# Kernel optimization log

Hardware: AMD Instinct MI355X
Metric: run time of the kernel (lower is better)

Reference implementation:

```python
import jax, jax.numpy as jnp
import numpy as np

NI, ND, NH = 128, 32, 4  # feature dim, head dim, n heads


def setup_inputs() -> dict:
    key = jax.random.key(0)
    ks = jax.random.split(key, 8)
    nb, nloc, nnei = 2, 1024, 120
    g1 = jax.random.normal(ks[0], (nb, nloc, NI), dtype=jnp.float32)
    gg1 = jax.random.normal(ks[1], (nb, nloc, nnei, NI), dtype=jnp.float32)
    nlist_mask = jax.random.randint(ks[2], (nb, nloc, nnei), 0, 2) > 0
    sw = jax.random.uniform(ks[3], (nb, nloc, nnei), dtype=jnp.float32)
    s = 1.0 / np.sqrt(NI)
    Wq = jax.random.normal(ks[4], (NI, ND * NH), dtype=jnp.float32) * s
    Wkv = jax.random.normal(ks[5], (NI, (ND + NI) * NH), dtype=jnp.float32) * s
    Wh = jax.random.normal(ks[6], (NI * NH, NI), dtype=jnp.float32) * (1.0 / np.sqrt(NI * NH))
    bh = jax.random.normal(ks[7], (NI,), dtype=jnp.float32) * 0.01
    return {"g1": g1, "gg1": gg1, "nlist_mask": nlist_mask, "sw": sw,
            "Wq": Wq, "Wkv": Wkv, "Wh": Wh, "bh": bh}


def reference(g1, gg1, nlist_mask, sw, Wq, Wkv, Wh, bh):
    nb, nloc, nnei = nlist_mask.shape
    # q: [nb, nloc, nh, nd]
    q = (g1 @ Wq).reshape(nb, nloc, ND, NH).transpose(0, 1, 3, 2)
    # kv: [nb, nloc, nh, nnei, nd+ni]
    kv = (gg1 @ Wkv).reshape(nb, nloc, nnei, ND + NI, NH).transpose(0, 1, 4, 2, 3)
    k = kv[..., :ND]   # [nb, nloc, nh, nnei, nd]
    v = kv[..., ND:]   # [nb, nloc, nh, nnei, ni]
    # attention logits over neighbors: [nb, nloc, nh, nnei]
    attnw = jnp.einsum("blhd,blhjd->blhj", q, k) / np.sqrt(ND).astype(np.float32)
    mask = nlist_mask[:, :, None, :]  # [nb, nloc, 1, nnei]
    attnw = jnp.where(mask, attnw, -jnp.inf)
    attnw = jax.nn.softmax(attnw, axis=-1)
    attnw = jnp.where(mask, attnw, 0.0)
    attnw = attnw * sw[:, :, None, :]  # smoothing weight
    ret = jnp.einsum("blhj,blhji->blhi", attnw, v).reshape(nb, nloc, NH * NI)
    return ret @ Wh + bh
```

## Files before the change

kernel.cpp:

```cpp
#include <hip/hip_runtime.h>
#include <math.h>

#define NI   128
#define ND   32
#define NH   4
#define NNEI 120
#define KVW  640
#define NCOL 512

template<int CTRL>
__device__ __forceinline__ float dppf(float x) {
    return __int_as_float(__builtin_amdgcn_update_dpp(
        0, __float_as_int(x), CTRL, 0xF, 0xF, true));
}
__device__ __forceinline__ float red16_sum(float x) {
    x += dppf<0xB1>(x);
    x += dppf<0x4E>(x);
    x += dppf<0x141>(x);
    x += dppf<0x140>(x);
    return x;
}
__device__ __forceinline__ float red16_max(float x) {
    x = fmaxf(x, dppf<0xB1>(x));
    x = fmaxf(x, dppf<0x4E>(x));
    x = fmaxf(x, dppf<0x141>(x));
    x = fmaxf(x, dppf<0x140>(x));
    return x;
}

__global__ __launch_bounds__(256)
void precompute_MP(const float* __restrict__ Wq, const float* __restrict__ Wkv,
                   const float* __restrict__ Wh, float* __restrict__ M2, float* __restrict__ P2)
{
    int idx = blockIdx.x * 256 + threadIdx.x;
    if (idx < NI * NCOL) {
        int i  = idx & 127;
        int h  = (idx >> 7) & 3;
        int i2 = idx >> 9;
        float acc = 0.f;
        #pragma unroll 8
        for (int d = 0; d < ND; ++d)
            acc += Wq[i2 * NI + d * NH + h] * Wkv[i * KVW + d * NH + h];
        M2[i2 * NCOL + h * NI + i] = acc * 0.17677669529663687f;
    } else {
        int j  = idx - NI * NCOL;
        int io = j & 127;
        int i  = (j >> 7) & 127;
        int h  = j >> 14;
        float acc = 0.f;
        #pragma unroll 8
        for (int iv = 0; iv < NI; ++iv)
            acc += Wkv[i * KVW + (ND + iv) * NH + h] * Wh[(h * NI + iv) * NI + io];
        P2[j] = acc;
    }
}

template<int BM, int BN, int BK, int TM, int TN, bool BIAS>
__global__ __launch_bounds__(256)
void gemm_kernel(const float* __restrict__ A, const float* __restrict__ B,
                 const float* __restrict__ bias, float* __restrict__ C,
                 int M, int N, int K)
{
    __shared__ float As[BK][BM + 4];
    __shared__ float Bs[BK][BN + 4];
    const int tid = threadIdx.x;
    const int nbx = N / BN;
    const int bx = blockIdx.x % nbx, by = blockIdx.x / nbx;
    const int m0 = by * BM, n0 = bx * BN;
    const int tx = tid & 15, ty = tid >> 4;

    constexpr int LA = BM * BK / (4 * 256);
    constexpr int LB = BK * BN / (4 * 256);
    constexpr int AF4 = BK / 4;
    constexpr int BF4 = BN / 4;

    float acc[TM][TN] = {};

    for (int k0 = 0; k0 < K; k0 += BK) {
        #pragma unroll
        for (int p = 0; p < LA; ++p) {
            int u  = tid + p * 256;
            int r  = u / AF4;
            int c4 = u % AF4;
            float4 v = *(const float4*)(A + (size_t)(m0 + r) * K + k0 + c4 * 4);
            As[c4 * 4 + 0][r] = v.x;
            As[c4 * 4 + 1][r] = v.y;
            As[c4 * 4 + 2][r] = v.z;
            As[c4 * 4 + 3][r] = v.w;
        }
        #pragma unroll
        for (int p = 0; p < LB; ++p) {
            int u  = tid + p * 256;
            int kk = u / BF4;
            int c4 = u % BF4;
            float4 v = *(const float4*)(B + (size_t)(k0 + kk) * N + n0 + c4 * 4);
            *(float4*)&Bs[kk][c4 * 4] = v;
        }
        __syncthreads();
        #pragma unroll
        for (int kk = 0; kk < BK; ++kk) {
            float a[TM], b[TN];
            if constexpr (TM == 4) {
                float4 a4 = *(const float4*)&As[kk][ty * 4];
                a[0] = a4.x; a[1] = a4.y; a[2] = a4.z; a[3] = a4.w;
            } else {
                #pragma unroll
                for (int m = 0; m < TM; ++m) a[m] = As[kk][ty * TM + m];
            }
            if constexpr (TN == 4) {
                float4 b4 = *(const float4*)&Bs[kk][tx * 4];
                b[0] = b4.x; b[1] = b4.y; b[2] = b4.z; b[3] = b4.w;
            } else {
                #pragma unroll
                for (int n = 0; n < TN; ++n) b[n] = Bs[kk][tx * TN + n];
            }
            #pragma unroll
            for (int m = 0; m < TM; ++m)
                #pragma unroll
                for (int n = 0; n < TN; ++n)
                    acc[m][n] += a[m] * b[n];
        }
        __syncthreads();
    }
    #pragma unroll
    for (int m = 0; m < TM; ++m) {
        int mm = m0 + ty * TM + m;
        #pragma unroll
        for (int n = 0; n < TN; ++n) {
            int nn = n0 + tx * TN + n;
            C[(size_t)mm * N + nn] = acc[m][n] + (BIAS ? bias[nn] : 0.f);
        }
    }
}

__device__ __forceinline__ bool load_mask(const void* p, int is_i32, int idx) {
    if (is_i32) return ((const int*)p)[idx] != 0;
    return ((const unsigned char*)p)[idx] != 0;
}

__global__ __launch_bounds__(256, 3)
void atten_kernel(const float* __restrict__ gg1, const float* __restrict__ qW_all,
                  const void* __restrict__ mask_raw, const float* __restrict__ sw,
                  const float* __restrict__ P2, const float* __restrict__ bh,
                  float* __restrict__ out)
{
    __shared__ float  s_sm[NH][NNEI];
    __shared__ float4 s_part2[16][NH][33];
    __shared__ float4 s_t4[NH][32];
    __shared__ int    s_is_i32;

    const int tid  = threadIdx.x;
    const int bl   = blockIdx.x;
    const int w    = tid >> 6;
    const int lane = tid & 63;
    const int q    = lane >> 4;
    const int c    = lane & 15;

    if (tid < 64) {
        unsigned v = ((const unsigned*)mask_raw)[tid];
        unsigned long long b = __ballot(v <= 1u);
        if (tid == 0) s_is_i32 = (b == 0xFFFFFFFFFFFFFFFFull) ? 1 : 0;
    }

    const int j0 = lane, j1 = lane + 64;
    const int j1c = (j1 < NNEI) ? j1 : 0;
    float sw0 = sw[bl * NNEI + j0];
    float sw1 = (j1 < NNEI) ? sw[bl * NNEI + j1] : 0.f;
    unsigned mraw0_i = ((const int*)mask_raw)[bl * NNEI + j0];
    unsigned mraw1_i = ((const int*)mask_raw)[bl * NNEI + j1c];
    unsigned mraw0_b = ((const unsigned char*)mask_raw)[bl * NNEI + j0];
    unsigned mraw1_b = ((const unsigned char*)mask_raw)[bl * NNEI + j1c];

    const float4* gbase = (const float4*)(gg1 + (size_t)bl * NNEI * NI);
    float4 rgA[8], rgB[8];
    #pragma unroll
    for (int t = 0; t < 8; ++t) {
        int j  = 16 * t + 4 * q + w;
        int jc = (j < NNEI) ? j : 0;
        rgA[t] = gbase[jc * 32 + c];
        rgB[t] = gbase[jc * 32 + c + 16];
    }

    const float4* qwbase = (const float4*)(qW_all + (size_t)bl * NCOL);
    float4 qwA[NH], qwB[NH];
    #pragma unroll
    for (int h = 0; h < NH; ++h) {
        qwA[h] = qwbase[h * 32 + c];
        qwB[h] = qwbase[h * 32 + c + 16];
    }

    #pragma unroll
    for (int t = 0; t < 8; ++t) {
        float4 gA = rgA[t], gB = rgB[t];
        float s0, s1, s2, s3;
        s0 = qwA[0].x*gA.x + qwA[0].y*gA.y + qwA[0].z*gA.z + qwA[0].w*gA.w
           + qwB[0].x*gB.x + qwB[0].y*gB.y + qwB[0].z*gB.z + qwB[0].w*gB.w;
        s1 = qwA[1].x*gA.x + qwA[1].y*gA.y + qwA[1].z*gA.z + qwA[1].w*gA.w
           + qwB[1].x*gB.x + qwB[1].y*gB.y + qwB[1].z*gB.z + qwB[1].w*gB.w;
        s2 = qwA[2].x*gA.x + qwA[2].y*gA.y + qwA[2].z*gA.z + qwA[2].w*gA.w
           + qwB[2].x*gB.x + qwB[2].y*gB.y + qwB[2].z*gB.z + qwB[2].w*gB.w;
        s3 = qwA[3].x*gA.x + qwA[3].y*gA.y + qwA[3].z*gA.z + qwA[3].w*gA.w
           + qwB[3].x*gB.x + qwB[3].y*gB.y + qwB[3].z*gB.z + qwB[3].w*gB.w;
        s0 = red16_sum(s0);
        s1 = red16_sum(s1);
        s2 = red16_sum(s2);
        s3 = red16_sum(s3);
        int j = 16 * t + 4 * q + w;
        if (c == 0 && j < NNEI) {
            s_sm[0][j] = s0;
            s_sm[1][j] = s1;
            s_sm[2][j] = s2;
            s_sm[3][j] = s3;
        }
    }
    __syncthreads();

    {
        const int is32 = s_is_i32;
        bool m0 = is32 ? (mraw0_i != 0u) : ((mraw0_b & 0xFFu) != 0u);
        bool m1 = (j1 < NNEI) && (is32 ? (mraw1_i != 0u) : ((mraw1_b & 0xFFu) != 0u));
        float v0 = m0 ? s_sm[w][j0] : -INFINITY;
        float v1 = m1 ? s_sm[w][j1c] : -INFINITY;

        float mx = fmaxf(v0, v1);
        mx = red16_max(mx);
        mx = fmaxf(mx, __shfl_xor(mx, 16));
        mx = fmaxf(mx, __shfl_xor(mx, 32));

        float e0 = 0.f, e1 = 0.f;
        if (mx != -INFINITY) {
            e0 = m0 ? __expf(v0 - mx) : 0.f;
            e1 = m1 ? __expf(v1 - mx) : 0.f;
        }
        float s = e0 + e1;
        s = red16_sum(s);
        s += __shfl_xor(s, 16);
        s += __shfl_xor(s, 32);
        float inv = (s > 0.f) ? (1.f / s) : 0.f;

        s_sm[w][j0] = e0 * inv * sw0;
        if (j1 < NNEI) s_sm[w][j1] = e1 * inv * sw1;
    }
    __syncthreads();

    {
        float4 aA[NH] = {}, aB[NH] = {};
        #pragma unroll
        for (int t = 0; t < 8; ++t) {
            int j = 16 * t + 4 * q + w;
            bool val = (j < NNEI);
            float4 gA = rgA[t], gB = rgB[t];
            #pragma unroll
            for (int h = 0; h < NH; ++h) {
                float a = val ? s_sm[h][j] : 0.f;
                aA[h].x += a * gA.x; aA[h].y += a * gA.y;
                aA[h].z += a * gA.z; aA[h].w += a * gA.w;
                aB[h].x += a * gB.x; aB[h].y += a * gB.y;
                aB[h].z += a * gB.z; aB[h].w += a * gB.w;
            }
        }
        #pragma unroll
        for (int h = 0; h < NH; ++h) {
            s_part2[w * 4 + q][h][c]      = aA[h];
            s_part2[w * 4 + q][h][c + 16] = aB[h];
        }
    }
    __syncthreads();

    if (tid < 128) {
        int h = tid >> 5, cc = tid & 31;
        float4 r = {0.f, 0.f, 0.f, 0.f};
        #pragma unroll
        for (int g = 0; g < 16; ++g) {
            float4 v = s_part2[g][h][cc];
            r.x += v.x; r.y += v.y; r.z += v.z; r.w += v.w;
        }
        s_t4[h][cc] = r;
    }
    __syncthreads();

    {
        const int io4 = tid & 31, g = tid >> 5;
        float4 oacc = {0.f, 0.f, 0.f, 0.f};
        const float4* P2_4 = (const float4*)P2;
        const float*  s_tf = (const float*)s_t4;
        #pragma unroll 8
        for (int it = 0; it < 64; ++it) {
            int kk = it * 8 + g;
            float4 p = P2_4[kk * 32 + io4];
            float tv = s_tf[kk];
            oacc.x += tv * p.x; oacc.y += tv * p.y;
            oacc.z += tv * p.z; oacc.w += tv * p.w;
        }
        float4* s_pp = &s_part2[0][0][0];
        s_pp[g * 33 + io4] = oacc;
    }
    __syncthreads();
    if (tid < 32) {
        const float4* s_pp = &s_part2[0][0][0];
        float4 r = {0.f, 0.f, 0.f, 0.f};
        #pragma unroll
        for (int g = 0; g < 8; ++g) {
            float4 v = s_pp[g * 33 + tid];
            r.x += v.x; r.y += v.y; r.z += v.z; r.w += v.w;
        }
        float4 b = ((const float4*)bh)[tid];
        r.x += b.x; r.y += b.y; r.z += b.z; r.w += b.w;
        ((float4*)out)[(size_t)bl * 32 + tid] = r;
    }
}

__global__ __launch_bounds__(256, 2)
void fused_fallback(const float* __restrict__ g1, const float* __restrict__ gg1,
                    const void* __restrict__ mask_raw, const float* __restrict__ sw,
                    const float* __restrict__ M2, const float* __restrict__ P2,
                    const float* __restrict__ bh, float* __restrict__ out)
{
    __shared__ float s_gg[NNEI * 129];
    __shared__ float s_qW[NH][NI];
    __shared__ float s_attn[NH][NNEI];
    __shared__ float s_t[NH][NI];
    __shared__ float s_part[2][NI];
    __shared__ int   s_is_i32;

    const int tid = threadIdx.x;
    const int bl  = blockIdx.x;

    if (tid < 64) {
        unsigned v = ((const unsigned*)mask_raw)[tid];
        unsigned long long b = __ballot(v <= 1u);
        if (tid == 0) s_is_i32 = (b == 0xFFFFFFFFFFFFFFFFull) ? 1 : 0;
    }
    {
        const float4* gsrc = (const float4*)(gg1 + (size_t)bl * NNEI * NI);
        #pragma unroll
        for (int p = 0; p < 15; ++p) {
            int u = tid + p * 256;
            int r = u >> 5, c4 = u & 31;
            float4 v = gsrc[u];
            float* dst = &s_gg[r * 129 + c4 * 4];
            dst[0] = v.x; dst[1] = v.y; dst[2] = v.z; dst[3] = v.w;
        }
    }
    {
        const float* g1r = g1 + bl * NI;
        #pragma unroll
        for (int p = 0; p < 2; ++p) {
            int o = tid + p * 256;
            int i = o & (NI - 1);
            int h = o >> 7;
            const float* Mp = M2 + h * NI + i;
            float acc = 0.f;
            #pragma unroll 8
            for (int i2 = 0; i2 < NI; ++i2) acc += g1r[i2] * Mp[i2 * NCOL];
            s_qW[h][i] = acc;
        }
    }
    __syncthreads();
    {
        const int lane = tid & 63, h = tid >> 6;
        const int j0 = lane, j1 = lane + 64;
        const int j1c = (j1 < NNEI) ? j1 : 0;
        const float* row0 = &s_gg[j0 * 129];
        const float* row1 = &s_gg[j1c * 129];
        float dot0 = 0.f, dot1 = 0.f;
        #pragma unroll 8
        for (int i = 0; i < NI; ++i) {
            float w = s_qW[h][i];
            dot0 += row0[i] * w;
            dot1 += row1[i] * w;
        }
        bool m0 = load_mask(mask_raw, s_is_i32, bl * NNEI + j0);
        bool m1 = (j1 < NNEI) && load_mask(mask_raw, s_is_i32, bl * NNEI + j1c);
        float v0 = m0 ? dot0 : -INFINITY;
        float v1 = m1 ? dot1 : -INFINITY;
        float mx = fmaxf(v0, v1);
        #pragma unroll
        for (int off = 32; off; off >>= 1) mx = fmaxf(mx, __shfl_xor(mx, off));
        float e0 = 0.f, e1 = 0.f;
        if (mx != -INFINITY) {
            e0 = m0 ? __expf(v0 - mx) : 0.f;
            e1 = m1 ? __expf(v1 - mx) : 0.f;
        }
        float s = e0 + e1;
        #pragma unroll
        for (int off = 32; off; off >>= 1) s += __shfl_xor(s, off);
        float inv = (s > 0.f) ? (1.f / s) : 0.f;
        s_attn[h][j0] = e0 * inv * sw[bl * NNEI + j0];
        if (j1 < NNEI) s_attn[h][j1] = e1 * inv * sw[bl * NNEI + j1];
    }
    __syncthreads();
    #pragma unroll
    for (int p = 0; p < 2; ++p) {
        int o = tid + p * 256;
        int i = o & (NI - 1);
        int h = o >> 7;
        float acc = 0.f;
        #pragma unroll 8
        for (int j = 0; j < NNEI; ++j) acc += s_attn[h][j] * s_gg[j * 129 + i];
        s_t[h][i] = acc;
    }
    __syncthreads();
    {
        int io = tid & (NI - 1);
        int half = tid >> 7;
        float acc = 0.f;
        #pragma unroll 2
        for (int h = half * 2; h < half * 2 + 2; ++h) {
            const float* Pp = P2 + h * NI * NI + io;
            #pragma unroll 8
            for (int i = 0; i < NI; ++i) acc += s_t[h][i] * Pp[i * NI];
        }
        s_part[half][io] = acc;
    }
    __syncthreads();
    if (tid < NI)
        out[bl * NI + tid] = s_part[0][tid] + s_part[1][tid] + bh[tid];
}

extern "C" void kernel_launch(void* const* d_in, const int* in_sizes, int n_in,
                              void* d_out, int out_size, void* d_ws, size_t ws_size,
                              hipStream_t stream) {
    const float* g1   = (const float*)d_in[0];
    const float* gg1  = (const float*)d_in[1];
    const void*  mask = d_in[2];
    const float* sw   = (const float*)d_in[3];
    const float* Wq   = (const float*)d_in[4];
    const float* Wkv  = (const float*)d_in[5];
    const float* Wh   = (const float*)d_in[6];
    const float* bh   = (const float*)d_in[7];
    float* out = (float*)d_out;

    const int nbl = in_sizes[0] / NI;
    const size_t nM = (size_t)NI * NCOL;
    const size_t nP = (size_t)NCOL * NI;
    const size_t nQ = (size_t)nbl * NCOL;

    float* M2 = (float*)d_ws;
    float* P2 = M2 + nM;

    precompute_MP<<<512, 256, 0, stream>>>(Wq, Wkv, Wh, M2, P2);

    if (ws_size >= (nM + nP + nQ) * sizeof(float)) {
        float* qW = P2 + nP;
        gemm_kernel<64, 64, 32, 4, 4, false>
            <<<(nbl / 64) * (NCOL / 64), 256, 0, stream>>>(g1, M2, nullptr, qW, nbl, NCOL, NI);
        atten_kernel<<<nbl, 256, 0, stream>>>(gg1, qW, mask, sw, P2, bh, out);
    } else {
        fused_fallback<<<nbl, 256, 0, stream>>>(g1, gg1, mask, sw, M2, P2, bh, out);
    }
}
```

Measured before the change: 56.52 us.

## Process two atoms per attention block and fuse P2 precompute into qW GEMM

The attention kernel now handles two atoms per block. Each P2 float4 load in the output projection is reused for both atoms, and the second atom's gg1 rows are loaded while the first is being reduced. The precompute is split: M2 gets its own small kernel, and the P2 computation moves into extra blocks of the qW GEMM launch so it runs alongside the GEMM. The cost is half as many attention blocks, which lowers parallelism across CUs, and the main path is now hard-coded to nbl==2048.

```diff
diff --git a/kernel.cpp b/kernel.cpp
--- a/kernel.cpp
+++ b/kernel.cpp
@@ -26,6 +26,21 @@
     x = fmaxf(x, dppf<0x141>(x));
     x = fmaxf(x, dppf<0x140>(x));
     return x;
+}
+
+__global__ __launch_bounds__(256)
+void precompute_M2(const float* __restrict__ Wq, const float* __restrict__ Wkv,
+                   float* __restrict__ M2)
+{
+    int idx = blockIdx.x * 256 + threadIdx.x;
+    int i  = idx & 127;
+    int h  = (idx >> 7) & 3;
+    int i2 = idx >> 9;
+    float acc = 0.f;
+    #pragma unroll 8
+    for (int d = 0; d < ND; ++d)
+        acc += Wq[i2 * NI + d * NH + h] * Wkv[i * KVW + d * NH + h];
+    M2[i2 * NCOL + h * NI + i] = acc * 0.17677669529663687f;
 }
 
 __global__ __launch_bounds__(256)
@@ -55,82 +70,86 @@
     }
 }
 
-template<int BM, int BN, int BK, int TM, int TN, bool BIAS>
+#define G1_BM 64
+#define G1_BN 64
+#define G1_BK 32
 __global__ __launch_bounds__(256)
-void gemm_kernel(const float* __restrict__ A, const float* __restrict__ B,
-                 const float* __restrict__ bias, float* __restrict__ C,
-                 int M, int N, int K)
-{
-    __shared__ float As[BK][BM + 4];
-    __shared__ float Bs[BK][BN + 4];
+void gemm1_p2(const float* __restrict__ g1, const float* __restrict__ M2,
+              const float* __restrict__ Wkv, const float* __restrict__ Wh,
+              float* __restrict__ qW, float* __restrict__ P2)
+{
+    __shared__ float As[G1_BK][G1_BM + 4];
+    __shared__ float Bs[G1_BK][G1_BN + 4];
     const int tid = threadIdx.x;
-    const int nbx = N / BN;
+
+    if (blockIdx.x >= 256) {
+        int j  = (blockIdx.x - 256) * 256 + tid;
+        int io = j & 127;
+        int i  = (j >> 7) & 127;
+        int h  = j >> 14;
+        float acc = 0.f;
+        #pragma unroll 8
+        for (int iv = 0; iv < NI; ++iv)
+            acc += Wkv[i * KVW + (ND + iv) * NH + h] * Wh[(h * NI + iv) * NI + io];
+        P2[j] = acc;
+        return;
+    }
+
+    const int nbx = NCOL / G1_BN;
     const int bx = blockIdx.x % nbx, by = blockIdx.x / nbx;
-    const int m0 = by * BM, n0 = bx * BN;
+    const int m0 = by * G1_BM, n0 = bx * G1_BN;
     const int tx = tid & 15, ty = tid >> 4;
-
-    constexpr int LA = BM * BK / (4 * 256);
-    constexpr int LB = BK * BN / (4 * 256);
-    constexpr int AF4 = BK / 4;
-    constexpr int BF4 = BN / 4;
-
-    float acc[TM][TN] = {};
-
-    for (int k0 = 0; k0 < K; k0 += BK) {
-        #pragma unroll
-        for (int p = 0; p < LA; ++p) {
-            int u  = tid + p * 256;
-            int r  = u / AF4;
-            int c4 = u % AF4;
-            float4 v = *(const float4*)(A + (size_t)(m0 + r) * K + k0 + c4 * 4);
-            As[c4 * 4 + 0][r] = v.x;
-            As[c4 * 4 + 1][r] = v.y;
-            As[c4 * 4 + 2][r] = v.z;
-            As[c4 * 4 + 3][r] = v.w;
-        }
-        #pragma unroll
-        for (int p = 0; p < LB; ++p) {
-            int u  = tid + p * 256;
-            int kk = u / BF4;
-            int c4 = u % BF4;
-            float4 v = *(const float4*)(B + (size_t)(k0 + kk) * N + n0 + c4 * 4);
-            *(float4*)&Bs[kk][c4 * 4] = v;
+    const int M = 2048, N = NCOL, K = NI;
+
+    float acc[4][4] = {};
+    for (int k0 = 0; k0 < K; k0 += G1_BK) {
+        {
+            int u  = tid * 2;
+            int r  = u >> 5;
+            #pragma unroll
+            for (int e = 0; e < 2; ++e) {
+                int uu = tid + e * 256;
+                int rr = uu >> 3, c4 = uu & 7;
+                float4 v = *(const float4*)(g1 + (size_t)(m0 + rr) * K + k0 + c4 * 4);
+                As[c4 * 4 + 0][rr] = v.x;
+                As[c4 * 4 + 1][rr] = v.y;
+                As[c4 * 4 + 2][rr] = v.z;
+                As[c4 * 4 + 3][rr] = v.w;
+            }
+            (void)r; (void)u;
+        }
+        {
+            #pragma unroll
+            for (int e = 0; e < 2; ++e) {
+                int uu = tid + e * 256;
+                int kk = uu >> 4, c4 = uu & 15;
+                float4 v = *(const float4*)(M2 + (size_t)(k0 + kk) * N + n0 + c4 * 4);
+                *(float4*)&Bs[kk][c4 * 4] = v;
+            }
         }
         __syncthreads();
         #pragma unroll
-        for (int kk = 0; kk < BK; ++kk) {
-            float a[TM], b[TN];
-            if constexpr (TM == 4) {
-                float4 a4 = *(const float4*)&As[kk][ty * 4];
-                a[0] = a4.x; a[1] = a4.y; a[2] = a4.z; a[3] = a4.w;
-            } else {
+        for (int kk = 0; kk < G1_BK; ++kk) {
+            float4 a4 = *(const float4*)&As[kk][ty * 4];
+            float4 b4 = *(const float4*)&Bs[kk][tx * 4];
+            float a[4] = {a4.x, a4.y, a4.z, a4.w};
+            float b[4] = {b4.x, b4.y, b4.z, b4.w};
+            #pragma unroll
+            for (int m = 0; m < 4; ++m)
                 #pragma unroll
-                for (int m = 0; m < TM; ++m) a[m] = As[kk][ty * TM + m];
-            }
-            if constexpr (TN == 4) {
-                float4 b4 = *(const float4*)&Bs[kk][tx * 4];
-                b[0] = b4.x; b[1] = b4.y; b[2] = b4.z; b[3] = b4.w;
-            } else {
-                #pragma unroll
-                for (int n = 0; n < TN; ++n) b[n] = Bs[kk][tx * TN + n];
-            }
-            #pragma unroll
-            for (int m = 0; m < TM; ++m)
-                #pragma unroll
-                for (int n = 0; n < TN; ++n)
+                for (int n = 0; n < 4; ++n)
                     acc[m][n] += a[m] * b[n];
         }
         __syncthreads();
     }
     #pragma unroll
-    for (int m = 0; m < TM; ++m) {
-        int mm = m0 + ty * TM + m;
-        #pragma unroll
-        for (int n = 0; n < TN; ++n) {
-            int nn = n0 + tx * TN + n;
-            C[(size_t)mm * N + nn] = acc[m][n] + (BIAS ? bias[nn] : 0.f);
-        }
-    }
+    for (int m = 0; m < 4; ++m) {
+        int mm = m0 + ty * 4 + m;
+        #pragma unroll
+        for (int n = 0; n < 4; ++n)
+            qW[(size_t)mm * N + n0 + tx * 4 + n] = acc[m][n];
+    }
+    (void)M;
 }
 
 __device__ __forceinline__ bool load_mask(const void* p, int is_i32, int idx) {
@@ -138,57 +157,22 @@
     return ((const unsigned char*)p)[idx] != 0;
 }
 
-__global__ __launch_bounds__(256, 3)
-void atten_kernel(const float* __restrict__ gg1, const float* __restrict__ qW_all,
-                  const void* __restrict__ mask_raw, const float* __restrict__ sw,
-                  const float* __restrict__ P2, const float* __restrict__ bh,
-                  float* __restrict__ out)
-{
-    __shared__ float  s_sm[NH][NNEI];
-    __shared__ float4 s_part2[16][NH][33];
-    __shared__ float4 s_t4[NH][32];
-    __shared__ int    s_is_i32;
-
-    const int tid  = threadIdx.x;
-    const int bl   = blockIdx.x;
-    const int w    = tid >> 6;
-    const int lane = tid & 63;
-    const int q    = lane >> 4;
-    const int c    = lane & 15;
-
-    if (tid < 64) {
-        unsigned v = ((const unsigned*)mask_raw)[tid];
-        unsigned long long b = __ballot(v <= 1u);
-        if (tid == 0) s_is_i32 = (b == 0xFFFFFFFFFFFFFFFFull) ? 1 : 0;
-    }
-
-    const int j0 = lane, j1 = lane + 64;
-    const int j1c = (j1 < NNEI) ? j1 : 0;
-    float sw0 = sw[bl * NNEI + j0];
-    float sw1 = (j1 < NNEI) ? sw[bl * NNEI + j1] : 0.f;
-    unsigned mraw0_i = ((const int*)mask_raw)[bl * NNEI + j0];
-    unsigned mraw1_i = ((const int*)mask_raw)[bl * NNEI + j1c];
-    unsigned mraw0_b = ((const unsigned char*)mask_raw)[bl * NNEI + j0];
-    unsigned mraw1_b = ((const unsigned char*)mask_raw)[bl * NNEI + j1c];
-
-    const float4* gbase = (const float4*)(gg1 + (size_t)bl * NNEI * NI);
-    float4 rgA[8], rgB[8];
+__device__ __forceinline__ void load_rows(const float4* gbase, int w, int q, int c,
+                                          float4 (&A)[8], float4 (&B)[8]) {
     #pragma unroll
     for (int t = 0; t < 8; ++t) {
         int j  = 16 * t + 4 * q + w;
         int jc = (j < NNEI) ? j : 0;
-        rgA[t] = gbase[jc * 32 + c];
-        rgB[t] = gbase[jc * 32 + c + 16];
-    }
-
-    const float4* qwbase = (const float4*)(qW_all + (size_t)bl * NCOL);
-    float4 qwA[NH], qwB[NH];
-    #pragma unroll
-    for (int h = 0; h < NH; ++h) {
-        qwA[h] = qwbase[h * 32 + c];
-        qwB[h] = qwbase[h * 32 + c + 16];
-    }
-
+        A[t] = gbase[jc * 32 + c];
+        B[t] = gbase[jc * 32 + c + 16];
+    }
+}
+
+__device__ __forceinline__ void phase1_logits(
+    const float4 (&rgA)[8], const float4 (&rgB)[8],
+    const float4 (&qwA)[NH], const float4 (&qwB)[NH],
+    float (*s_sm)[NNEI], int w, int q, int c)
+{
     #pragma unroll
     for (int t = 0; t < 8; ++t) {
         float4 gA = rgA[t], gB = rgB[t];
@@ -213,60 +197,66 @@
             s_sm[3][j] = s3;
         }
     }
-    __syncthreads();
-
-    {
-        const int is32 = s_is_i32;
-        bool m0 = is32 ? (mraw0_i != 0u) : ((mraw0_b & 0xFFu) != 0u);
-        bool m1 = (j1 < NNEI) && (is32 ? (mraw1_i != 0u) : ((mraw1_b & 0xFFu) != 0u));
-        float v0 = m0 ? s_sm[w][j0] : -INFINITY;
-        float v1 = m1 ? s_sm[w][j1c] : -INFINITY;
-
-        float mx = fmaxf(v0, v1);
-        mx = red16_max(mx);
-        mx = fmaxf(mx, __shfl_xor(mx, 16));
-        mx = fmaxf(mx, __shfl_xor(mx, 32));
-
-        float e0 = 0.f, e1 = 0.f;
-        if (mx != -INFINITY) {
-            e0 = m0 ? __expf(v0 - mx) : 0.f;
-            e1 = m1 ? __expf(v1 - mx) : 0.f;
-        }
-        float s = e0 + e1;
-        s = red16_sum(s);
-        s += __shfl_xor(s, 16);
-        s += __shfl_xor(s, 32);
-        float inv = (s > 0.f) ? (1.f / s) : 0.f;
-
-        s_sm[w][j0] = e0 * inv * sw0;
-        if (j1 < NNEI) s_sm[w][j1] = e1 * inv * sw1;
-    }
-    __syncthreads();
-
-    {
-        float4 aA[NH] = {}, aB[NH] = {};
-        #pragma unroll
-        for (int t = 0; t < 8; ++t) {
-            int j = 16 * t + 4 * q + w;
-            bool val = (j < NNEI);
-            float4 gA = rgA[t], gB = rgB[t];
-            #pragma unroll
-            for (int h = 0; h < NH; ++h) {
-                float a = val ? s_sm[h][j] : 0.f;
-                aA[h].x += a * gA.x; aA[h].y += a * gA.y;
-                aA[h].z += a * gA.z; aA[h].w += a * gA.w;
-                aB[h].x += a * gB.x; aB[h].y += a * gB.y;
-                aB[h].z += a * gB.z; aB[h].w += a * gB.w;
-            }
-        }
+}
+
+__device__ __forceinline__ void softmax_inplace(
+    float (*s_sm)[NNEI], int w, int lane,
+    bool m0, bool m1, float sw0, float sw1)
+{
+    const int j0 = lane, j1 = lane + 64;
+    const int j1c = (j1 < NNEI) ? j1 : 0;
+    float v0 = m0 ? s_sm[w][j0] : -INFINITY;
+    float v1 = m1 ? s_sm[w][j1c] : -INFINITY;
+
+    float mx = fmaxf(v0, v1);
+    mx = red16_max(mx);
+    mx = fmaxf(mx, __shfl_xor(mx, 16));
+    mx = fmaxf(mx, __shfl_xor(mx, 32));
+
+    float e0 = 0.f, e1 = 0.f;
+    if (mx != -INFINITY) {
+        e0 = m0 ? __expf(v0 - mx) : 0.f;
+        e1 = m1 ? __expf(v1 - mx) : 0.f;
+    }
+    float s = e0 + e1;
+    s = red16_sum(s);
+    s += __shfl_xor(s, 16);
+    s += __shfl_xor(s, 32);
+    float inv = (s > 0.f) ? (1.f / s) : 0.f;
+
+    s_sm[w][j0] = e0 * inv * sw0;
+    if (j1 < NNEI) s_sm[w][j1] = e1 * inv * sw1;
+}
+
+__device__ __forceinline__ void phase2_partial(
+    const float4 (&rgA)[8], const float4 (&rgB)[8],
+    float (*s_sm)[NNEI], float4 (*s_part2)[NH][33], int w, int q, int c)
+{
+    float4 aA[NH] = {}, aB[NH] = {};
+    #pragma unroll
+    for (int t = 0; t < 8; ++t) {
+        int j = 16 * t + 4 * q + w;
+        bool val = (j < NNEI);
+        float4 gA = rgA[t], gB = rgB[t];
         #pragma unroll
         for (int h = 0; h < NH; ++h) {
-            s_part2[w * 4 + q][h][c]      = aA[h];
-            s_part2[w * 4 + q][h][c + 16] = aB[h];
-        }
-    }
-    __syncthreads();
-
+            float a = val ? s_sm[h][j] : 0.f;
+            aA[h].x += a * gA.x; aA[h].y += a * gA.y;
+            aA[h].z += a * gA.z; aA[h].w += a * gA.w;
+            aB[h].x += a * gB.x; aB[h].y += a * gB.y;
+            aB[h].z += a * gB.z; aB[h].w += a * gB.w;
+        }
+    }
+    #pragma unroll
+    for (int h = 0; h < NH; ++h) {
+        s_part2[w * 4 + q][h][c]      = aA[h];
+        s_part2[w * 4 + q][h][c + 16] = aB[h];
+    }
+}
+
+__device__ __forceinline__ void fold_t(
+    const float4 (*s_part2)[NH][33], float4 (*s_t4a)[32], int tid)
+{
     if (tid < 128) {
         int h = tid >> 5, cc = tid & 31;
         float4 r = {0.f, 0.f, 0.f, 0.f};
@@ -275,38 +265,126 @@
             float4 v = s_part2[g][h][cc];
             r.x += v.x; r.y += v.y; r.z += v.z; r.w += v.w;
         }
-        s_t4[h][cc] = r;
-    }
+        s_t4a[h][cc] = r;
+    }
+}
+
+__global__ __launch_bounds__(256, 3)
+void atten2_kernel(const float* __restrict__ gg1, const float* __restrict__ qW_all,
+                   const void* __restrict__ mask_raw, const float* __restrict__ sw,
+                   const float* __restrict__ P2, const float* __restrict__ bh,
+                   float* __restrict__ out)
+{
+    __shared__ float  s_sm[NH][NNEI];
+    __shared__ float4 s_part2[16][NH][33];
+    __shared__ float4 s_t4[2][NH][32];
+    __shared__ int    s_is_i32;
+
+    const int tid  = threadIdx.x;
+    const int bl0  = blockIdx.x * 2;
+    const int bl1  = bl0 + 1;
+    const int w    = tid >> 6;
+    const int lane = tid & 63;
+    const int q    = lane >> 4;
+    const int c    = lane & 15;
+    const int j0   = lane, j1 = lane + 64;
+    const int j1c  = (j1 < NNEI) ? j1 : 0;
+
+    if (tid < 64) {
+        unsigned v = ((const unsigned*)mask_raw)[tid];
+        unsigned long long b = __ballot(v <= 1u);
+        if (tid == 0) s_is_i32 = (b == 0xFFFFFFFFFFFFFFFFull) ? 1 : 0;
+    }
+
+    float sw0_0 = sw[bl0 * NNEI + j0];
+    float sw1_0 = (j1 < NNEI) ? sw[bl0 * NNEI + j1] : 0.f;
+    unsigned a0mi0 = ((const int*)mask_raw)[bl0 * NNEI + j0];
+    unsigned a0mi1 = ((const int*)mask_raw)[bl0 * NNEI + j1c];
+    unsigned a0mb0 = ((const unsigned char*)mask_raw)[bl0 * NNEI + j0];
+    unsigned a0mb1 = ((const unsigned char*)mask_raw)[bl0 * NNEI + j1c];
+
+    const float4* gb0 = (const float4*)(gg1 + (size_t)bl0 * NNEI * NI);
+    const float4* gb1 = (const float4*)(gg1 + (size_t)bl1 * NNEI * NI);
+    float4 rgA[8], rgB[8];
+    load_rows(gb0, w, q, c, rgA, rgB);
+
+    const float4* qwb0 = (const float4*)(qW_all + (size_t)bl0 * NCOL);
+    float4 qwA[NH], qwB[NH];
+    #pragma unroll
+    for (int h = 0; h < NH; ++h) {
+        qwA[h] = qwb0[h * 32 + c];
+        qwB[h] = qwb0[h * 32 + c + 16];
+    }
+
+    phase1_logits(rgA, rgB, qwA, qwB, s_sm, w, q, c);
+    __syncthreads();
+    const int is32 = s_is_i32;
+    {
+        bool m0 = is32 ? (a0mi0 != 0u) : (a0mb0 != 0u);
+        bool m1 = (j1 < NNEI) && (is32 ? (a0mi1 != 0u) : (a0mb1 != 0u));
+        softmax_inplace(s_sm, w, lane, m0, m1, sw0_0, sw1_0);
+    }
+    __syncthreads();
+    phase2_partial(rgA, rgB, s_sm, s_part2, w, q, c);
+
+    load_rows(gb1, w, q, c, rgA, rgB);
+    const float4* qwb1 = (const float4*)(qW_all + (size_t)bl1 * NCOL);
+    #pragma unroll
+    for (int h = 0; h < NH; ++h) {
+        qwA[h] = qwb1[h * 32 + c];
+        qwB[h] = qwb1[h * 32 + c + 16];
+    }
+    bool a1m0 = load_mask(mask_raw, is32, bl1 * NNEI + j0);
+    bool a1m1 = (j1 < NNEI) && load_mask(mask_raw, is32, bl1 * NNEI + j1c);
+    float sw0_1 = sw[bl1 * NNEI + j0];
+    float sw1_1 = (j1 < NNEI) ? sw[bl1 * NNEI + j1] : 0.f;
+
+    __syncthreads();
+    fold_t(s_part2, s_t4[0], tid);
+    __syncthreads();
+
+    phase1_logits(rgA, rgB, qwA, qwB, s_sm, w, q, c);
+    __syncthreads();
+    softmax_inplace(s_sm, w, lane, a1m0, a1m1, sw0_1, sw1_1);
+    __syncthreads();
+    phase2_partial(rgA, rgB, s_sm, s_part2, w, q, c);
+    __syncthreads();
+    fold_t(s_part2, s_t4[1], tid);
     __syncthreads();
 
     {
         const int io4 = tid & 31, g = tid >> 5;
-        float4 oacc = {0.f, 0.f, 0.f, 0.f};
+        float4 o0 = {0.f, 0.f, 0.f, 0.f};
+        float4 o1 = {0.f, 0.f, 0.f, 0.f};
         const float4* P2_4 = (const float4*)P2;
-        const float*  s_tf = (const float*)s_t4;
+        const float* t0f = (const float*)&s_t4[0][0][0];
+        const float* t1f = (const float*)&s_t4[1][0][0];
         #pragma unroll 8
         for (int it = 0; it < 64; ++it) {
             int kk = it * 8 + g;
             float4 p = P2_4[kk * 32 + io4];
-            float tv = s_tf[kk];
-            oacc.x += tv * p.x; oacc.y += tv * p.y;
-            oacc.z += tv * p.z; oacc.w += tv * p.w;
+            float tv0 = t0f[kk];
+            float tv1 = t1f[kk];
+            o0.x += tv0 * p.x; o0.y += tv0 * p.y; o0.z += tv0 * p.z; o0.w += tv0 * p.w;
+            o1.x += tv1 * p.x; o1.y += tv1 * p.y; o1.z += tv1 * p.z; o1.w += tv1 * p.w;
         }
         float4* s_pp = &s_part2[0][0][0];
-        s_pp[g * 33 + io4] = oacc;
-    }
-    __syncthreads();
-    if (tid < 32) {
+        s_pp[g * 33 + io4]       = o0;
+        s_pp[264 + g * 33 + io4] = o1;
+    }
+    __syncthreads();
+    if (tid < 64) {
+        int a = tid >> 5, io4 = tid & 31;
         const float4* s_pp = &s_part2[0][0][0];
         float4 r = {0.f, 0.f, 0.f, 0.f};
         #pragma unroll
         for (int g = 0; g < 8; ++g) {
-            float4 v = s_pp[g * 33 + tid];
+            float4 v = s_pp[a * 264 + g * 33 + io4];
             r.x += v.x; r.y += v.y; r.z += v.z; r.w += v.w;
         }
-        float4 b = ((const float4*)bh)[tid];
+        float4 b = ((const float4*)bh)[io4];
         r.x += b.x; r.y += b.y; r.z += b.z; r.w += b.w;
-        ((float4*)out)[(size_t)bl * 32 + tid] = r;
+        ((float4*)out)[(size_t)(bl0 + a) * 32 + io4] = r;
     }
 }
 
@@ -439,14 +517,16 @@
     float* M2 = (float*)d_ws;
     float* P2 = M2 + nM;
 
-    precompute_MP<<<512, 256, 0, stream>>>(Wq, Wkv, Wh, M2, P2);
-
-    if (ws_size >= (nM + nP + nQ) * sizeof(float)) {
+    const bool main_path = (ws_size >= (nM + nP + nQ) * sizeof(float)) &&
+                           (nbl == 2048);
+
+    if (main_path) {
         float* qW = P2 + nP;
-        gemm_kernel<64, 64, 32, 4, 4, false>
-            <<<(nbl / 64) * (NCOL / 64), 256, 0, stream>>>(g1, M2, nullptr, qW, nbl, NCOL, NI);
-        atten_kernel<<<nbl, 256, 0, stream>>>(gg1, qW, mask, sw, P2, bh, out);
+        precompute_M2<<<256, 256, 0, stream>>>(Wq, Wkv, M2);
+        gemm1_p2<<<512, 256, 0, stream>>>(g1, M2, Wkv, Wh, qW, P2);
+        atten2_kernel<<<nbl / 2, 256, 0, stream>>>(gg1, qW, mask, sw, P2, bh, out);
     } else {
+        precompute_MP<<<512, 256, 0, stream>>>(Wq, Wkv, Wh, M2, P2);
         fused_fallback<<<nbl, 256, 0, stream>>>(g1, gg1, mask, sw, M2, P2, bh, out);
     }
 }
```

Result: faster. 52.00 us (-8.0%).
